# Performance work log

Hardware: AMD Instinct MI355X
Metric: run time of the kernel (lower is better)

The kernel has to match this reference:

```python
import jax, jax.numpy as jnp
import numpy as np
from jax import lax

G, K, KS = 4, 16, 3            # stripes, latents per stripe, support kernel
TEMP, TOPK_RATIO, GATE, EPS = 0.125, 0.125, 0.05, 1e-6


def _l2norm(v):
    # F.normalize(p=2, dim=-1): divide by max(norm, 1e-12)
    return v / jnp.maximum(jnp.linalg.norm(v, axis=-1, keepdims=True), 1e-12)


def _avg_pool3(x):
    # 3x3 avg pool, stride 1, pad 1, count_include_pad=True (torch default)
    s = lax.reduce_window(x, 0.0, lax.add, (1, 1, KS, KS), (1, 1, 1, 1),
                          [(0, 0), (0, 0), (KS // 2, KS // 2), (KS // 2, KS // 2)])
    return s / float(KS * KS)


def setup_inputs() -> dict:
    key = jax.random.key(0)
    k1, k2 = jax.random.split(key)
    x = jax.random.normal(k1, (64, 256, 64, 44), dtype=jnp.float32)
    latent_basis = jax.random.normal(k2, (G, K, 256), dtype=jnp.float32) * 0.05
    return {"x": x, "latent_basis": latent_basis}


def reference(x, latent_basis):
    n, c, h, w = x.shape
    hs = h // G
    # 'n c (g hs) w -> (n g) c hs w'
    sf = x.reshape(n, c, G, hs, w).transpose(0, 2, 1, 3, 4).reshape(n * G, c, hs, w)
    support_feat = _avg_pool3(sf)
    feat_flat = sf.reshape(n, G, c, hs * w).transpose(0, 1, 3, 2)          # n g p c
    supp_flat = support_feat.reshape(n, G, c, hs * w).transpose(0, 1, 3, 2)  # n g p c
    # active mask from detached energy
    e = jnp.mean(lax.stop_gradient(sf) ** 2, axis=1)                       # [n*G, hs, w]
    e = e / jnp.maximum(jnp.max(e, axis=(-2, -1), keepdims=True), EPS)
    am = (e > GATE).astype(jnp.float32)
    fb = (e > 0).astype(jnp.float32)
    use_fb = jnp.sum(am, axis=(-2, -1), keepdims=True) <= 0
    am = jnp.where(use_fb, fb, am).reshape(n, G, hs * w)                   # n g p
    # routing
    sfn = _l2norm(supp_flat)
    lb = _l2norm(latent_basis)                                             # g k c
    logits = jnp.einsum('ngpc,gkc->ngpk', sfn, lb) / TEMP
    route = jax.nn.softmax(logits, axis=-1)
    supp = route * am[..., None]                                           # n g p k
    pw = supp / jnp.maximum(jnp.sum(supp, axis=2, keepdims=True), EPS)
    tokens = jnp.einsum('ngpk,ngpc->ngkc', pw, feat_flat)                  # n g k c
    tokens = tokens.transpose(0, 3, 1, 2).reshape(n, c, G * K)             # n c (g k)
    # presence via top-k over positions
    p = supp.shape[2]
    topk = max(1, min(p, int(p * TOPK_RATIO)))
    vals = lax.top_k(supp.transpose(0, 1, 3, 2), topk)[0]                  # n g k topk
    pres = jnp.mean(vals, axis=-1).reshape(n, G * K)
    pres = pres / jnp.maximum(jnp.sum(pres, axis=1, keepdims=True), EPS)
    return tokens, pres
```

## Files before the change

kernel.cpp:

```cpp
#include <hip/hip_runtime.h>
#include <cstdint>


#define C_ 256
#define W_ 44
#define P_ 704
#define CH_STRIDE 2816
#define NB_STRIDE 720896
#define TOPK_ 88
#define GATE_ 0.05f
#define EPS_ 1e-6f

#define DPP_WAVE_SHL1 0x130
#define DPP_WAVE_SHR1 0x138
__device__ __forceinline__ float dpp_from_left(float v) {
  return __int_as_float(__builtin_amdgcn_update_dpp(
      0, __float_as_int(v), DPP_WAVE_SHR1, 0xF, 0xF, true));
}
__device__ __forceinline__ float dpp_from_right(float v) {
  return __int_as_float(__builtin_amdgcn_update_dpp(
      0, __float_as_int(v), DPP_WAVE_SHL1, 0xF, 0xF, true));
}

__global__ __launch_bounds__(256) void k_norm_basis(const float* __restrict__ lb,
                                                    float* __restrict__ lbn) {
  int gk = blockIdx.x;
  int t = threadIdx.x;
  float v = lb[gk * 256 + t];
  float ss = v * v;
  #pragma unroll
  for (int off = 32; off >= 1; off >>= 1) ss += __shfl_xor(ss, off);
  __shared__ float red[4];
  if ((t & 63) == 0) red[t >> 6] = ss;
  __syncthreads();
  float tot = red[0] + red[1] + red[2] + red[3];
  float scale = 1.f / fmaxf(sqrtf(tot), 1e-12f);
  int g = gk >> 4, k = gk & 15;
  lbn[((g * 256 + t) << 4) + k] = v * scale;
}

#define LOAD_GRP(Pm, P0, Pp, cbase)                                    \
  { _Pragma("unroll")                                                  \
    for (int j_ = 0; j_ < 4; j_++) {                                   \
      const size_t o_ = (size_t)((cbase) + j_) * CH_STRIDE;            \
      Pm[j_] = xm[o_]; P0[j_] = xb[o_]; Pp[j_] = xp[o_];               \
    } }

#define CONS_GRP(Pm, P0, Pp, cbase)                                    \
  { _Pragma("unroll")                                                  \
    for (int j_ = 0; j_ < 4; j_++) {                                   \
      float a  = act ? P0[j_] : 0.f;                                   \
      float am_ = (act && hm) ? Pm[j_] : 0.f;                          \
      float ap_ = (act && hp) ? Pp[j_] : 0.f;                          \
      float vs = am_ + a + ap_;                                        \
      float lf = dpp_from_left(vs);                                    \
      float rt = dpp_from_right(vs);                                   \
      float win = lf + vs + rt;                                        \
      pw2 = fmaf(win, win, pw2);                                       \
      sq  = fmaf(a, a, sq);                                            \
      const int co_ = __builtin_amdgcn_readfirstlane(((cbase) + j_) << 4); \
      const float4* wp4 = (const float4*)(lbb + co_);                  \
      float4 w0 = wp4[0], w1 = wp4[1], w2 = wp4[2], w3 = wp4[3];       \
      rawdot[0]  = fmaf(a, w0.x, rawdot[0]);  rawdot[1]  = fmaf(a, w0.y, rawdot[1]);  \
      rawdot[2]  = fmaf(a, w0.z, rawdot[2]);  rawdot[3]  = fmaf(a, w0.w, rawdot[3]);  \
      rawdot[4]  = fmaf(a, w1.x, rawdot[4]);  rawdot[5]  = fmaf(a, w1.y, rawdot[5]);  \
      rawdot[6]  = fmaf(a, w1.z, rawdot[6]);  rawdot[7]  = fmaf(a, w1.w, rawdot[7]);  \
      rawdot[8]  = fmaf(a, w2.x, rawdot[8]);  rawdot[9]  = fmaf(a, w2.y, rawdot[9]);  \
      rawdot[10] = fmaf(a, w2.z, rawdot[10]); rawdot[11] = fmaf(a, w2.w, rawdot[11]); \
      rawdot[12] = fmaf(a, w3.x, rawdot[12]); rawdot[13] = fmaf(a, w3.y, rawdot[13]); \
      rawdot[14] = fmaf(a, w3.z, rawdot[14]); rawdot[15] = fmaf(a, w3.w, rawdot[15]); \
    } }

__global__ __launch_bounds__(1024, 4) void k_route(const float* __restrict__ x,
                                                   const float* __restrict__ lbn,
                                                   float* __restrict__ supp_pk,
                                                   float* __restrict__ invden_ws,
                                                   float* __restrict__ presraw) {
  __shared__ float rsl[11264];
  __shared__ uint32_t hist_l[16 * 256];
  __shared__ float redA[16];
  __shared__ float redB[16];
  __shared__ float redM[2];
  __shared__ float red2[16 * 16];

  const int tid = threadIdx.x;
  const int w = tid >> 6;
  const int l = tid & 63;
  const bool act = (l < 44);
  const int s = blockIdx.x, n = s >> 2, g = s & 3;
  const int p = w * 44 + l;

  const int lsafe = act ? l : 0;
  const float* xb = x + (size_t)n * NB_STRIDE + (g * 16 + w) * 44 + lsafe;
  const float* xm = xb + ((w > 0)  ? -44 : 0);
  const float* xp = xb + ((w < 15) ?  44 : 0);
  const bool hm = (w > 0), hp = (w < 15);

  const float* lbb = lbn + (g << 12);

  float rawdot[16];
  #pragma unroll
  for (int k = 0; k < 16; k++) rawdot[k] = 0.f;
  float sq = 0.f, pw2 = 0.f;

  float Avm[4], Av0[4], Avp[4];
  float Bvm[4], Bv0[4], Bvp[4];

  LOAD_GRP(Avm, Av0, Avp, 0)
  for (int c = 0; c < 256; c += 8) {
    LOAD_GRP(Bvm, Bv0, Bvp, c + 4)
    CONS_GRP(Avm, Av0, Avp, c)
    if (c + 8 < 256) { LOAD_GRP(Avm, Av0, Avp, c + 8) }
    CONS_GRP(Bvm, Bv0, Bvp, c + 4)
  }

  if (act) {
    #pragma unroll
    for (int k = 0; k < 16; k++) rsl[k * 704 + p] = rawdot[k];
  }
  __syncthreads();

  float pd[16];
  #pragma unroll
  for (int k = 0; k < 16; k++) pd[k] = 0.f;
  if (act) {
    #pragma unroll
    for (int dy = -1; dy <= 1; dy++) {
      int yy = w + dy;
      if (yy < 0 || yy > 15) continue;
      #pragma unroll
      for (int dx = -1; dx <= 1; dx++) {
        int xx = l + dx;
        if (xx < 0 || xx > 43) continue;
        int pp = yy * 44 + xx;
        #pragma unroll
        for (int k = 0; k < 16; k++) pd[k] += rsl[k * 704 + pp];
      }
    }
  }

  float e_raw = sq * (1.f / 256.f);
  float m = e_raw;
  #pragma unroll
  for (int off = 32; off >= 1; off >>= 1) m = fmaxf(m, __shfl_xor(m, off));
  if (l == 0) redA[w] = m;
  __syncthreads();
  if (tid == 0) {
    float mm = redA[0];
    for (int w2 = 1; w2 < 16; w2++) mm = fmaxf(mm, redA[w2]);
    redM[0] = mm;
  }
  __syncthreads();
  float M = fmaxf(redM[0], EPS_);
  float e = e_raw / M;
  float am = (e > GATE_) ? 1.f : 0.f;
  float fb = (e_raw > 0.f) ? 1.f : 0.f;
  float a = am;
  #pragma unroll
  for (int off = 32; off >= 1; off >>= 1) a += __shfl_xor(a, off);
  if (l == 0) redB[w] = a;
  __syncthreads();
  if (tid == 0) {
    float sm = 0.f;
    for (int w2 = 0; w2 < 16; w2++) sm += redB[w2];
    redM[1] = sm;
  }
  __syncthreads();
  if (redM[1] <= 0.f) am = fb;

  float pnorm = sqrtf(pw2) * (1.f / 9.f);
  float invn = 1.f / fmaxf(pnorm, 1e-12f);
  float scl = invn * (8.f / 9.f);
  float li[16];
  float mx = -1e30f;
  #pragma unroll
  for (int k = 0; k < 16; k++) { li[k] = pd[k] * scl; mx = fmaxf(mx, li[k]); }
  float ssum = 0.f;
  #pragma unroll
  for (int k = 0; k < 16; k++) { li[k] = __expf(li[k] - mx); ssum += li[k]; }
  float rs2 = am / ssum;
  float supp[16];
  #pragma unroll
  for (int k = 0; k < 16; k++) supp[k] = li[k] * rs2;

  if (act) {
    float* spk = supp_pk + ((size_t)s * 704 + p) * 16;
    #pragma unroll
    for (int kq = 0; kq < 4; kq++)
      ((float4*)spk)[kq] = make_float4(supp[kq*4+0], supp[kq*4+1],
                                       supp[kq*4+2], supp[kq*4+3]);
  }

  #pragma unroll
  for (int k = 0; k < 16; k++) {
    float v2 = act ? supp[k] : 0.f;
    #pragma unroll
    for (int off = 32; off >= 1; off >>= 1) v2 += __shfl_xor(v2, off);
    if (l == 0) red2[w * 16 + k] = v2;
  }
  __syncthreads();
  if (tid < 16) {
    float den = 0.f;
    for (int w2 = 0; w2 < 16; w2++) den += red2[w2 * 16 + tid];
    invden_ws[s * 16 + tid] = 1.f / fmaxf(den, EPS_);
  }

  if (act) {
    #pragma unroll
    for (int k = 0; k < 16; k++) rsl[k * 704 + p] = supp[k];
  }
  __syncthreads();

  {
    const int k = w;
    uint32_t key[11];
    #pragma unroll
    for (int j = 0; j < 11; j++)
      key[j] = __float_as_uint(rsl[k * 704 + l + 64 * j]);
    uint32_t* h = &hist_l[w * 256];
    uint32_t prefix = 0, remaining = TOPK_;
    #pragma unroll
    for (int b = 3; b >= 0; b--) {
      const int shift = b * 8;
      *(uint4*)&h[l * 4] = make_uint4(0u, 0u, 0u, 0u);
      uint32_t mhi = (b == 3) ? 0u : (0xFFFFFFFFu << (shift + 8));
      #pragma unroll
      for (int j = 0; j < 11; j++)
        if ((key[j] & mhi) == (prefix & mhi))
          atomicAdd(&h[(key[j] >> shift) & 255u], 1u);
      uint4 bn = *(uint4*)&h[l * 4];
      uint32_t T = bn.x + bn.y + bn.z + bn.w;
      uint32_t inc = T;
      #pragma unroll
      for (int off = 1; off < 64; off <<= 1) {
        uint32_t o = (uint32_t)__shfl_down((int)inc, off);
        if (l + off < 64) inc += o;
      }
      uint32_t excl = inc - T;
      uint32_t g3 = excl + bn.w, g2 = g3 + bn.z, g1 = g2 + bn.y, g0 = g1 + bn.x;
      uint32_t pk = 0u;
      if (g0 >= remaining && g1 < remaining) pk = ((uint32_t)(4*l+0) << 16) | (remaining - g1);
      if (g1 >= remaining && g2 < remaining) pk = ((uint32_t)(4*l+1) << 16) | (remaining - g2);
      if (g2 >= remaining && g3 < remaining) pk = ((uint32_t)(4*l+2) << 16) | (remaining - g3);
      if (g3 >= remaining && excl < remaining) pk = ((uint32_t)(4*l+3) << 16) | (remaining - excl);
      #pragma unroll
      for (int off = 32; off >= 1; off >>= 1) pk |= (uint32_t)__shfl_xor((int)pk, off);
      prefix |= ((pk >> 16) & 255u) << shift;
      remaining = pk & 0xFFFFu;
    }
    float tf = __uint_as_float(prefix);
    float sgt = 0.f; uint32_t cgt = 0u;
    #pragma unroll
    for (int j = 0; j < 11; j++)
      if (key[j] > prefix) { sgt += __uint_as_float(key[j]); cgt++; }
    #pragma unroll
    for (int off = 32; off >= 1; off >>= 1) {
      sgt += __shfl_xor(sgt, off);
      cgt += (uint32_t)__shfl_xor((int)cgt, off);
    }
    if (l == 0)
      presraw[s * 16 + k] = (sgt + (float)(TOPK_ - cgt) * tf) * (1.f / (float)TOPK_);
  }
}

__global__ __launch_bounds__(512, 4) void k_tokens(const float* __restrict__ x,
                                                   const float* __restrict__ supp_pk,
                                                   const float* __restrict__ invden,
                                                   float* __restrict__ out) {
  __shared__ float xl[4096];
  __shared__ float sl[11264];
  const int tid = threadIdx.x;
  const int bid = blockIdx.x;
  const int s = bid >> 1, chalf = bid & 1;
  const int n = s >> 2, g = s & 3;
  const int cl = tid & 127;
  const int q = tid >> 7;

  const float* xs = x + (size_t)n * NB_STRIDE + (size_t)(chalf * 128) * CH_STRIDE + g * P_;

  const int li0 = tid, li1 = tid + 512;
  const int lc0 = li0 >> 3, lj0 = li0 & 7;
  const int lc1 = li1 >> 3, lj1 = li1 & 7;
  const float* gp0 = xs + (size_t)lc0 * CH_STRIDE + lj0 * 4;
  const float* gp1 = xs + (size_t)lc1 * CH_STRIDE + lj1 * 4;
  const int wo0 = lc0 * 32 + ((lj0 * 4) ^ ((lc0 & 7) * 4));
  const int wo1 = lc1 * 32 + ((lj1 * 4) ^ ((lc1 & 7) * 4));

  const int sw = (cl & 7) * 4;
  const int rbase = cl * 32;

  float acc[16];
  #pragma unroll
  for (int k = 0; k < 16; k++) acc[k] = 0.f;

  {
    const float4* ssrc = (const float4*)(supp_pk + (size_t)s * 11264);
    float4* sdst = (float4*)sl;
    #pragma unroll
    for (int i = 0; i < 6; i++) {
      int idx = tid + i * 512;
      if (idx < 2816) sdst[idx] = ssrc[idx];
    }
  }
  float4 r0 = *(const float4*)gp0;
  float4 r1 = *(const float4*)gp1;
  *(float4*)&xl[wo0] = r0;
  *(float4*)&xl[wo1] = r1;
  __syncthreads();

  for (int tt = 0; tt < 22; tt++) {
    const int p0 = tt * 32;
    float4 n0, n1;
    if (tt < 21) {
      n0 = *(const float4*)(gp0 + p0 + 32);
      n1 = *(const float4*)(gp1 + p0 + 32);
    }

    #pragma unroll
    for (int jj = 0; jj < 8; jj += 4) {
      const int pp0 = q * 8 + jj;
      float4 xv = *(const float4*)&xl[rbase + (pp0 ^ sw)];
      float xa[4] = {xv.x, xv.y, xv.z, xv.w};
      #pragma unroll
      for (int dj = 0; dj < 4; dj++) {
        const float4* sp = (const float4*)&sl[(p0 + pp0 + dj) * 16];
        float4 s0 = sp[0], s1 = sp[1], s2 = sp[2], s3 = sp[3];
        float a = xa[dj];
        acc[0]  += a * s0.x; acc[1]  += a * s0.y; acc[2]  += a * s0.z; acc[3]  += a * s0.w;
        acc[4]  += a * s1.x; acc[5]  += a * s1.y; acc[6]  += a * s1.z; acc[7]  += a * s1.w;
        acc[8]  += a * s2.x; acc[9]  += a * s2.y; acc[10] += a * s2.z; acc[11] += a * s2.w;
        acc[12] += a * s3.x; acc[13] += a * s3.y; acc[14] += a * s3.z; acc[15] += a * s3.w;
      }
    }

    __syncthreads();
    if (tt < 21) {
      *(float4*)&xl[wo0] = n0;
      *(float4*)&xl[wo1] = n1;
      __syncthreads();
    }
  }

  if (q >= 2) {
    float* dst = &xl[((q - 2) * 128 + cl) * 16];
    #pragma unroll
    for (int kq = 0; kq < 4; kq++)
      ((float4*)dst)[kq] = make_float4(acc[kq*4], acc[kq*4+1], acc[kq*4+2], acc[kq*4+3]);
  }
  __syncthreads();
  if (q < 2) {
    const float* src = &xl[(q * 128 + cl) * 16];
    #pragma unroll
    for (int k = 0; k < 16; k++) acc[k] += src[k];
  }
  __syncthreads();
  if (q == 1) {
    float* dst = &xl[cl * 16];
    #pragma unroll
    for (int kq = 0; kq < 4; kq++)
      ((float4*)dst)[kq] = make_float4(acc[kq*4], acc[kq*4+1], acc[kq*4+2], acc[kq*4+3]);
  }
  __syncthreads();
  if (q == 0) {
    const float* src = &xl[cl * 16];
    float* op = out + ((size_t)(n * 256 + chalf * 128 + cl) * 64) + g * 16;
    #pragma unroll
    for (int kq = 0; kq < 4; kq++) {
      int u = __builtin_amdgcn_readfirstlane(s * 16 + kq * 4);
      const float4 iv = *(const float4*)(invden + u);
      float4 o;
      o.x = (acc[kq*4+0] + src[kq*4+0]) * iv.x;
      o.y = (acc[kq*4+1] + src[kq*4+1]) * iv.y;
      o.z = (acc[kq*4+2] + src[kq*4+2]) * iv.z;
      o.w = (acc[kq*4+3] + src[kq*4+3]) * iv.w;
      ((float4*)op)[kq] = o;
    }
  }
}

__global__ __launch_bounds__(64) void k_pres(const float* __restrict__ presraw,
                                             float* __restrict__ out) {
  const int n = blockIdx.x, t = threadIdx.x;
  float v = presraw[n * 64 + t];
  float ssum = v;
  #pragma unroll
  for (int off = 32; off >= 1; off >>= 1) ssum += __shfl_xor(ssum, off);
  out[1048576 + n * 64 + t] = v / fmaxf(ssum, EPS_);
}

extern "C" void kernel_launch(void* const* d_in, const int* in_sizes, int n_in,
                              void* d_out, int out_size, void* d_ws, size_t ws_size,
                              hipStream_t stream) {
  (void)in_sizes; (void)n_in; (void)out_size; (void)ws_size;
  const float* x  = (const float*)d_in[0];
  const float* lb = (const float*)d_in[1];
  float* out = (float*)d_out;
  float* ws = (float*)d_ws;
  float* lbn_ws     = ws;
  float* invden_ws  = ws + 16384;
  float* presraw_ws = ws + 20480;
  float* supp_pk_ws = ws + 2908160;

  k_norm_basis<<<64, 256, 0, stream>>>(lb, lbn_ws);
  k_route<<<256, 1024, 0, stream>>>(x, lbn_ws, supp_pk_ws, invden_ws, presraw_ws);
  k_tokens<<<512, 512, 0, stream>>>(x, supp_pk_ws, invden_ws, out);
  k_pres<<<64, 64, 0, stream>>>(presraw_ws, out);
}
```

Baseline: 330.3 us.

## Split token accumulation over position halves with separate reduction kernel

Each k_tokens block now handles half of the positions, doubling the grid to 1024 blocks and halving the support tile in shared memory. Partial token sums go to workspace, and a new k_tok_red kernel adds the two halves and applies the inverse denominator. This aims to raise occupancy and parallelism on the GPU. The cost is an extra launch and a partials write and read through global memory.

```diff
diff --git a/kernel.cpp b/kernel.cpp
--- a/kernel.cpp
+++ b/kernel.cpp
@@ -265,18 +265,20 @@
 
 __global__ __launch_bounds__(512, 4) void k_tokens(const float* __restrict__ x,
                                                    const float* __restrict__ supp_pk,
-                                                   const float* __restrict__ invden,
-                                                   float* __restrict__ out) {
+                                                   float* __restrict__ partials) {
   __shared__ float xl[4096];
-  __shared__ float sl[11264];
+  __shared__ float sl[5632];
   const int tid = threadIdx.x;
   const int bid = blockIdx.x;
-  const int s = bid >> 1, chalf = bid & 1;
+  const int s = bid >> 2;
+  const int chalf = (bid >> 1) & 1;
+  const int ph = bid & 1;
   const int n = s >> 2, g = s & 3;
   const int cl = tid & 127;
   const int q = tid >> 7;
 
-  const float* xs = x + (size_t)n * NB_STRIDE + (size_t)(chalf * 128) * CH_STRIDE + g * P_;
+  const float* xs = x + (size_t)n * NB_STRIDE + (size_t)(chalf * 128) * CH_STRIDE
+                      + g * P_ + ph * 352;
 
   const int li0 = tid, li1 = tid + 512;
   const int lc0 = li0 >> 3, lj0 = li0 & 7;
@@ -294,12 +296,12 @@
   for (int k = 0; k < 16; k++) acc[k] = 0.f;
 
   {
-    const float4* ssrc = (const float4*)(supp_pk + (size_t)s * 11264);
+    const float4* ssrc = (const float4*)(supp_pk + (size_t)s * 11264 + ph * 5632);
     float4* sdst = (float4*)sl;
     #pragma unroll
-    for (int i = 0; i < 6; i++) {
+    for (int i = 0; i < 3; i++) {
       int idx = tid + i * 512;
-      if (idx < 2816) sdst[idx] = ssrc[idx];
+      if (idx < 1408) sdst[idx] = ssrc[idx];
     }
   }
   float4 r0 = *(const float4*)gp0;
@@ -308,10 +310,10 @@
   *(float4*)&xl[wo1] = r1;
   __syncthreads();
 
-  for (int tt = 0; tt < 22; tt++) {
+  for (int tt = 0; tt < 11; tt++) {
     const int p0 = tt * 32;
     float4 n0, n1;
-    if (tt < 21) {
+    if (tt < 10) {
       n0 = *(const float4*)(gp0 + p0 + 32);
       n1 = *(const float4*)(gp1 + p0 + 32);
     }
@@ -334,7 +336,7 @@
     }
 
     __syncthreads();
-    if (tt < 21) {
+    if (tt < 10) {
       *(float4*)&xl[wo0] = n0;
       *(float4*)&xl[wo1] = n1;
       __syncthreads();
@@ -363,19 +365,40 @@
   __syncthreads();
   if (q == 0) {
     const float* src = &xl[cl * 16];
-    float* op = out + ((size_t)(n * 256 + chalf * 128 + cl) * 64) + g * 16;
+    float* op = partials + ((size_t)((s * 2 + chalf) * 2 + ph)) * 2048 + cl * 16;
     #pragma unroll
     for (int kq = 0; kq < 4; kq++) {
-      int u = __builtin_amdgcn_readfirstlane(s * 16 + kq * 4);
-      const float4 iv = *(const float4*)(invden + u);
       float4 o;
-      o.x = (acc[kq*4+0] + src[kq*4+0]) * iv.x;
-      o.y = (acc[kq*4+1] + src[kq*4+1]) * iv.y;
-      o.z = (acc[kq*4+2] + src[kq*4+2]) * iv.z;
-      o.w = (acc[kq*4+3] + src[kq*4+3]) * iv.w;
+      o.x = acc[kq*4+0] + src[kq*4+0];
+      o.y = acc[kq*4+1] + src[kq*4+1];
+      o.z = acc[kq*4+2] + src[kq*4+2];
+      o.w = acc[kq*4+3] + src[kq*4+3];
       ((float4*)op)[kq] = o;
     }
   }
+}
+
+__global__ __launch_bounds__(256) void k_tok_red(const float* __restrict__ partials,
+                                                 const float* __restrict__ invden,
+                                                 float* __restrict__ out) {
+  const int o4 = blockIdx.x * 256 + threadIdx.x;
+  const int f = o4 * 4;
+  const int n = f >> 14;
+  const int ch = (f >> 6) & 255;
+  const int r = f & 63;
+  const int g = r >> 4, k0 = r & 15;
+  const int s = n * 4 + g;
+  const int chalf = ch >> 7, cl = ch & 127;
+  const size_t b0 = ((size_t)((s * 2 + chalf) * 2 + 0)) * 2048 + cl * 16 + k0;
+  const float4 p0 = *(const float4*)(partials + b0);
+  const float4 p1 = *(const float4*)(partials + b0 + 2048);
+  const float4 iv = *(const float4*)(invden + s * 16 + k0);
+  float4 o;
+  o.x = (p0.x + p1.x) * iv.x;
+  o.y = (p0.y + p1.y) * iv.y;
+  o.z = (p0.z + p1.z) * iv.z;
+  o.w = (p0.w + p1.w) * iv.w;
+  *(float4*)(out + f) = o;
 }
 
 __global__ __launch_bounds__(64) void k_pres(const float* __restrict__ presraw,
@@ -399,10 +422,12 @@
   float* lbn_ws     = ws;
   float* invden_ws  = ws + 16384;
   float* presraw_ws = ws + 20480;
+  float* partial_ws = ws + 24576;
   float* supp_pk_ws = ws + 2908160;
 
   k_norm_basis<<<64, 256, 0, stream>>>(lb, lbn_ws);
   k_route<<<256, 1024, 0, stream>>>(x, lbn_ws, supp_pk_ws, invden_ws, presraw_ws);
-  k_tokens<<<512, 512, 0, stream>>>(x, supp_pk_ws, invden_ws, out);
+  k_tokens<<<1024, 512, 0, stream>>>(x, supp_pk_ws, partial_ws);
+  k_tok_red<<<1024, 256, 0, stream>>>(partial_ws, invden_ws, out);
   k_pres<<<64, 64, 0, stream>>>(presraw_ws, out);
 }
```

After: 330.0 us. About the same (-0.1%).
